# Kernel optimization log

Hardware: AMD Instinct MI355X
Metric: run time of the kernel (lower is better)

The kernel has to match this reference:

```python
import jax, jax.numpy as jnp
import numpy as np

B, L, D, H = 4, 8192, 512, 8


def _phi(x):
    # feature map: elu(x) + 1 (strictly positive)
    return jax.nn.elu(x) + 1.0


def setup_inputs() -> dict:
    key = jax.random.key(0)
    k1, k2, k3 = jax.random.split(key, 3)
    x = jax.random.normal(k1, (B, L, D), dtype=jnp.float32)
    w_qkv = jax.random.normal(k2, (D, 3 * D), dtype=jnp.float32) * 0.02
    b_qkv = jnp.zeros((3 * D,), dtype=jnp.float32)
    w_out = jax.random.normal(k3, (D, D), dtype=jnp.float32) * 0.02
    b_out = jnp.zeros((D,), dtype=jnp.float32)
    return {"x": x, "w_qkv": w_qkv, "b_qkv": b_qkv, "w_out": w_out,
            "b_out": b_out, "num_heads": H}


def reference(x, w_qkv, b_qkv, w_out, b_out, num_heads):
    Bx, Lx, Dx = x.shape
    dh = Dx // num_heads
    qkv = x @ w_qkv + b_qkv                       # (B, L, 3D)
    q, k, v = jnp.split(qkv, 3, axis=-1)
    # (B, L, D) -> (B, H, L, dh)
    def to_heads(t):
        return t.reshape(Bx, Lx, num_heads, dh).transpose(0, 2, 1, 3)
    q = _phi(to_heads(q))
    k = _phi(to_heads(k))
    v = to_heads(v)
    # kv[b,h,m,d] = sum_l k[b,h,l,d] * v[b,h,l,m]
    kv = jnp.einsum('bhld,bhlm->bhmd', k, v)      # (B, H, dh, dh)
    k_sum = jnp.sum(k, axis=2, keepdims=True)     # (B, H, 1, dh)
    # z[b,h,l,1] = 1 / <q_l, k_sum + 1e-6>
    z = 1.0 / jnp.einsum('bhld,bhmd->bhlm', q, k_sum + 1e-6)  # (B,H,L,1)
    out = jnp.einsum('bhld,bhmd->bhlm', q, kv) * z            # (B,H,L,dh)
    out = out.transpose(0, 2, 1, 3).reshape(Bx, Lx, Dx)
    return out @ w_out + b_out
```

## Files before the change

kernel.cpp:

```cpp
#include <hip/hip_runtime.h>
#include <hip/hip_bf16.h>
#include <math.h>

#define BB 4
#define LL 8192
#define DD 512
#define HH 8
#define MM (BB*LL)
#define NQKV 1536
#define CH 32

typedef __attribute__((ext_vector_type(4))) float f32x4;
typedef __attribute__((ext_vector_type(8))) short s16x8;
typedef __attribute__((ext_vector_type(4))) short s16x4;

__device__ __forceinline__ float bf2f(short u) {
  union { unsigned int i; float f; } c;
  c.i = ((unsigned int)(unsigned short)u) << 16;
  return c.f;
}
__device__ __forceinline__ short f2bf(float f) {
  union { float f; unsigned int i; } c; c.f = f;
  unsigned int r = c.i + 0x7FFFu + ((c.i >> 16) & 1u);
  return (short)(r >> 16);
}

__device__ __forceinline__ void gload16(const void* g, void* l) {
  __builtin_amdgcn_global_load_lds(
      (const __attribute__((address_space(1))) void*)(g),
      (__attribute__((address_space(3))) void*)(l), 16, 0, 0);
}

__global__ void conv_bf16(const float* __restrict__ in, short* __restrict__ out, int n) {
  int i = (blockIdx.x * blockDim.x + threadIdx.x) * 4;
  if (i < n) {
    float4 v = *reinterpret_cast<const float4*>(in + i);
    s16x4 o;
    o[0] = f2bf(v.x); o[1] = f2bf(v.y); o[2] = f2bf(v.z); o[3] = f2bf(v.w);
    *reinterpret_cast<s16x4*>(out + i) = o;
  }
}

__global__ void conv_wt(const float* __restrict__ w, short* __restrict__ wt, int K, int N) {
  int idx = blockIdx.x * blockDim.x + threadIdx.x;
  if (idx < K * N) {
    int n = idx / K, k = idx - n * K;
    wt[idx] = f2bf(w[(size_t)k * N + n]);
  }
}

template<int MODE>
__global__ __launch_bounds__(512, 4)
void gemm_bt(const short* __restrict__ A, const short* __restrict__ BT,
             const float* __restrict__ bias, void* __restrict__ Cout,
             short* __restrict__ ktb, short* __restrict__ vtb)
{
  constexpr int KD = 512;
  __shared__ __align__(16) char lds[65536];

  const int tid = threadIdx.x;
  const int wv = tid >> 6, lane = tid & 63;
  const int wm = wv >> 1, wn = wv & 1;
  const int fr = lane & 15, fq = lane >> 4;

  const int gx = gridDim.x;
  const int gy = gridDim.y;
  const int d = blockIdx.y * gx + blockIdx.x;
  const int nwg = gx * gy;
  const int lin = (d & 7) * (nwg >> 3) + (d >> 3);
  const int m0 = (lin / gy) * 256, n0 = (lin % gy) * 128;

  const int srow = tid >> 3;
  const int sunit = (tid & 7) ^ (srow & 7);
  const short* Ag = A  + (size_t)(m0 + srow) * KD + sunit * 8;
  const short* Bg = BT + (size_t)(n0 + srow) * KD + sunit * 8;
  char* ldsw = lds + wv * 1024;

  f32x4 acc[4][4] = {};

  for (int t = 0; t < 8; ++t) {
    const int k0 = t * 64;
#pragma unroll
    for (int i = 0; i < 4; ++i)
      gload16(Ag + (size_t)(i * 64) * KD + k0, ldsw + i * 8192);
#pragma unroll
    for (int i = 0; i < 2; ++i)
      gload16(Bg + (size_t)(i * 64) * KD + k0, ldsw + 32768 + i * 8192);
    __syncthreads();
#pragma unroll
    for (int kk = 0; kk < 2; ++kk) {
      s16x8 af[4], bfg[4];
#pragma unroll
      for (int i = 0; i < 4; ++i) {
        const int ra = wm * 64 + i * 16 + fr;
        const int ua = (kk * 4 + fq) ^ (ra & 7);
        af[i] = *(const s16x8*)(lds + ra * 128 + ua * 16);
      }
#pragma unroll
      for (int j = 0; j < 4; ++j) {
        const int rb = wn * 64 + j * 16 + fr;
        const int ub = (kk * 4 + fq) ^ (rb & 7);
        bfg[j] = *(const s16x8*)(lds + 32768 + rb * 128 + ub * 16);
      }
#pragma unroll
      for (int i = 0; i < 4; ++i)
#pragma unroll
        for (int j = 0; j < 4; ++j)
          acc[i][j] = __builtin_amdgcn_mfma_f32_16x16x32_bf16(af[i], bfg[j], acc[i][j], 0, 0, 0);
    }
    __syncthreads();
  }

  if (MODE == 0) {
    if (n0 < 512) {
      short* scr = (short*)lds;
#pragma unroll
      for (int j = 0; j < 4; ++j) {
        const int col = wn * 64 + j * 16 + fr;
        const float bv = bias[n0 + col];
#pragma unroll
        for (int i = 0; i < 4; ++i) {
          const int row = wm * 64 + i * 16 + fq * 4;
#pragma unroll
          for (int r = 0; r < 4; ++r) {
            float v = acc[i][j][r] + bv;
            v = (v > 0.f) ? (v + 1.f) : __expf(v);
            scr[(row + r) * 128 + col] = f2bf(v);
          }
        }
      }
      __syncthreads();
#pragma unroll
      for (int p = 0; p < 8; ++p) {
        const int off = p * 8192 + tid * 16;
        const int row = off >> 8, colb = off & 255;
        s16x8 v = *(const s16x8*)(lds + off);
        *(s16x8*)((short*)Cout + (size_t)(m0 + row) * 512 + n0 + (colb >> 1)) = v;
      }
    } else {
      const bool do_phi = (n0 < 1024);
      short* tdst = do_phi ? ktb : vtb;
      const int f0 = n0 - (do_phi ? 512 : 1024);
#pragma unroll
      for (int j = 0; j < 4; ++j) {
        const int col = wn * 64 + j * 16 + fr;
        const float bv = bias[n0 + col];
        const int cx = col & 31;
#pragma unroll
        for (int i = 0; i < 4; ++i) {
          const int l = wm * 64 + i * 16 + fq * 4;
          s16x4 pk;
#pragma unroll
          for (int r = 0; r < 4; ++r) {
            float v = acc[i][j][r] + bv;
            if (do_phi) v = (v > 0.f) ? (v + 1.f) : __expf(v);
            pk[r] = f2bf(v);
          }
          *(s16x4*)(lds + col * 512 + (((l >> 3) ^ cx) * 16) + (l & 7) * 2) = pk;
        }
      }
      __syncthreads();
#pragma unroll
      for (int p = 0; p < 8; ++p) {
        const int g = p * 512 + tid;
        const int col = g >> 5, up = g & 31;
        const int u = up ^ (col & 31);
        s16x8 v = *(const s16x8*)(lds + col * 512 + up * 16);
        const int f = f0 + col;
        const int hb = ((m0 >> 13) << 3) + (f >> 6);
        short* dst = tdst + ((size_t)hb * 64 + (f & 63)) * 8192 + (m0 & 8191) + u * 8;
        *(s16x8*)dst = v;
      }
    }
  } else {
    float* scrf = (float*)lds;
#pragma unroll
    for (int h = 0; h < 2; ++h) {
      __syncthreads();
      if ((wm >> 1) == h) {
#pragma unroll
        for (int j = 0; j < 4; ++j) {
          const int col = wn * 64 + j * 16 + fr;
          const float bv = bias[n0 + col];
#pragma unroll
          for (int i = 0; i < 4; ++i) {
            const int row = (wm & 1) * 64 + i * 16 + fq * 4;
#pragma unroll
            for (int r = 0; r < 4; ++r)
              scrf[(row + r) * 128 + col] = acc[i][j][r] + bv;
          }
        }
      }
      __syncthreads();
#pragma unroll
      for (int p = 0; p < 8; ++p) {
        const int off = p * 8192 + tid * 16;
        const int row = off >> 9, colb = off & 511;
        float4 v = *(const float4*)(lds + off);
        *(float4*)((float*)Cout + (size_t)(m0 + h * 128 + row) * 512 + n0 + (colb >> 2)) = v;
      }
    }
  }
}

__global__ __launch_bounds__(256, 4)
void kv_mfma(const short* __restrict__ kt, const short* __restrict__ vt,
             float* __restrict__ pkv, float* __restrict__ pks)
{
  const int hb = blockIdx.x, c = blockIdx.y;
  const int tid = threadIdx.x, wv = tid >> 6, lane = tid & 63;
  const int fr = lane & 15, fq = lane >> 4;
  const size_t base = (size_t)hb * 64 * 8192;
  const int l0 = c * 256;
  const short* vrow = vt + base + (size_t)fr * 8192 + l0 + fq * 8;
  const short* krow = kt + base + (size_t)(wv * 16 + fr) * 8192 + l0 + fq * 8;

  s16x8 ones;
#pragma unroll
  for (int j = 0; j < 8; ++j) ones[j] = (short)0x3F80;

  f32x4 acc[4] = {};
  f32x4 accd = {};
#pragma unroll
  for (int ks = 0; ks < 8; ++ks) {
    s16x8 bfr = *(const s16x8*)(krow + ks * 32);
    accd = __builtin_amdgcn_mfma_f32_16x16x32_bf16(ones, bfr, accd, 0, 0, 0);
#pragma unroll
    for (int i = 0; i < 4; ++i) {
      s16x8 af = *(const s16x8*)(vrow + (size_t)(i * 16) * 8192 + ks * 32);
      acc[i] = __builtin_amdgcn_mfma_f32_16x16x32_bf16(af, bfr, acc[i], 0, 0, 0);
    }
  }
  float* o = pkv + ((size_t)hb * CH + c) * 4096;
#pragma unroll
  for (int i = 0; i < 4; ++i)
#pragma unroll
    for (int r = 0; r < 4; ++r)
      o[(i * 16 + fq * 4 + r) * 64 + wv * 16 + fr] = acc[i][r];
  if (fq == 0)
    pks[((size_t)hb * CH + c) * 64 + wv * 16 + fr] = accd[0];
}

__global__ void kv_reduce(const float* __restrict__ pkv, const float* __restrict__ pks,
                          short* __restrict__ kv_b, short* __restrict__ ksum_b)
{
  const int idx = blockIdx.x * 256 + threadIdx.x;
  const int head = idx >> 12, md = idx & 4095;
  float s = 0.f;
  for (int i = 0; i < CH; ++i) s += pkv[((size_t)head * CH + i) * 4096 + md];
  kv_b[idx] = f2bf(s);
  if (md < 64) {
    float t = 0.f;
    for (int i = 0; i < CH; ++i) t += pks[((size_t)head * CH + i) * 64 + md];
    ksum_b[head * 64 + md] = f2bf(t + 1e-6f);
  }
}

__global__ __launch_bounds__(256, 2)
void attn_mfma(const short* __restrict__ q_b, const short* __restrict__ kv_b,
               const short* __restrict__ ksum_b, short* __restrict__ attn)
{
  const int hb = blockIdx.x;
  const int tile = blockIdx.y;
  const int b = hb >> 3, h = hb & 7;
  const int tid = threadIdx.x, wv = tid >> 6, lane = tid & 63;
  const int fr = lane & 15, fk = (lane >> 4) * 8;

  const short* kvp = kv_b + (size_t)hb * 4096;
  s16x8 bfrag[4][2];
#pragma unroll
  for (int j = 0; j < 4; ++j)
#pragma unroll
    for (int kk = 0; kk < 2; ++kk)
      bfrag[j][kk] = *(const s16x8*)(kvp + (j * 16 + fr) * 64 + kk * 32 + fk);
  s16x8 bden[2];
#pragma unroll
  for (int kk = 0; kk < 2; ++kk)
    bden[kk] = *(const s16x8*)(ksum_b + hb * 64 + kk * 32 + fk);

  const short* qb = q_b + (size_t)b * LL * DD + h * 64;
  const int l0 = tile * 256 + wv * 64;
  f32x4 accn[4][4] = {};
  f32x4 accd[4] = {};
#pragma unroll
  for (int i = 0; i < 4; ++i) {
#pragma unroll
    for (int kk = 0; kk < 2; ++kk) {
      s16x8 a = *(const s16x8*)(qb + (size_t)(l0 + i * 16 + fr) * DD + kk * 32 + fk);
      accd[i] = __builtin_amdgcn_mfma_f32_16x16x32_bf16(a, bden[kk], accd[i], 0, 0, 0);
#pragma unroll
      for (int j = 0; j < 4; ++j)
        accn[i][j] = __builtin_amdgcn_mfma_f32_16x16x32_bf16(a, bfrag[j][kk], accn[i][j], 0, 0, 0);
    }
  }

  short* ob = attn + (size_t)b * LL * DD + h * 64;
  const int fq = lane >> 4;
#pragma unroll
  for (int i = 0; i < 4; ++i) {
#pragma unroll
    for (int r = 0; r < 4; ++r) {
      const int row = l0 + i * 16 + fq * 4 + r;
      const float dinv = 1.0f / accd[i][r];
#pragma unroll
      for (int j = 0; j < 4; ++j) {
        ob[(size_t)row * DD + j * 16 + fr] = f2bf(accn[i][j][r] * dinv);
      }
    }
  }
}

extern "C" void kernel_launch(void* const* d_in, const int* in_sizes, int n_in,
                              void* d_out, int out_size, void* d_ws, size_t ws_size,
                              hipStream_t stream)
{
  const float* x     = (const float*)d_in[0];
  const float* w_qkv = (const float*)d_in[1];
  const float* b_qkv = (const float*)d_in[2];
  const float* w_out = (const float*)d_in[3];
  const float* b_out = (const float*)d_in[4];

  char* ws = (char*)d_ws;
  size_t off = 0;
  short* x_b   = (short*)(ws + off); off += (size_t)MM * DD * 2;
  short* wq_t  = (short*)(ws + off); off += (size_t)NQKV * DD * 2;
  short* wo_t  = (short*)(ws + off); off += (size_t)DD * DD * 2;
  short* q_b   = (short*)(ws + off); off += (size_t)MM * DD * 2;
  short* kt    = (short*)(ws + off); off += (size_t)32 * 64 * LL * 2;
  short* vt    = (short*)(ws + off); off += (size_t)32 * 64 * LL * 2;
  short* attn_b= (short*)(ws + off); off += (size_t)MM * DD * 2;
  float* pkv   = (float*)(ws + off); off += (size_t)32 * CH * 4096 * 4;
  float* pks   = (float*)(ws + off); off += (size_t)32 * CH * 64 * 4;
  short* kv_b  = (short*)(ws + off); off += (size_t)32 * 4096 * 2;
  short* ksum_b= (short*)(ws + off); off += (size_t)32 * 64 * 2;

  conv_bf16<<<dim3((MM * DD / 4 + 255) / 256), dim3(256), 0, stream>>>(x, x_b, MM * DD);
  conv_wt<<<dim3((DD * NQKV + 255) / 256), dim3(256), 0, stream>>>(w_qkv, wq_t, DD, NQKV);
  conv_wt<<<dim3((DD * DD + 255) / 256), dim3(256), 0, stream>>>(w_out, wo_t, DD, DD);

  gemm_bt<0><<<dim3(MM / 256, NQKV / 128), dim3(512), 0, stream>>>(
      x_b, wq_t, b_qkv, (void*)q_b, kt, vt);

  kv_mfma<<<dim3(32, CH), dim3(256), 0, stream>>>(kt, vt, pkv, pks);
  kv_reduce<<<dim3(512), dim3(256), 0, stream>>>(pkv, pks, kv_b, ksum_b);

  attn_mfma<<<dim3(32, 32), dim3(256), 0, stream>>>(q_b, kv_b, ksum_b, attn_b);

  gemm_bt<1><<<dim3(MM / 256, DD / 128), dim3(512), 0, stream>>>(
      attn_b, wo_t, b_out, d_out, nullptr, nullptr);
}
```

Measured before the change: 171.5 us.

## Enlarge GEMM tiles to 256x256 with a multi-stage LDS prefetch pipeline

```diff
diff --git a/kernel.cpp b/kernel.cpp
--- a/kernel.cpp
+++ b/kernel.cpp
@@ -50,64 +50,66 @@
 }
 
 template<int MODE>
-__global__ __launch_bounds__(512, 4)
-void gemm_bt(const short* __restrict__ A, const short* __restrict__ BT,
+__global__ __launch_bounds__(512, 2)
+void gemm256(const short* __restrict__ A, const short* __restrict__ BT,
              const float* __restrict__ bias, void* __restrict__ Cout,
              short* __restrict__ ktb, short* __restrict__ vtb)
 {
   constexpr int KD = 512;
-  __shared__ __align__(16) char lds[65536];
+  constexpr int NT = KD / 32;
+  __shared__ __align__(16) char lds[131072];
 
   const int tid = threadIdx.x;
   const int wv = tid >> 6, lane = tid & 63;
-  const int wm = wv >> 1, wn = wv & 1;
+  const int wm = wv >> 2, wn = wv & 3;
   const int fr = lane & 15, fq = lane >> 4;
 
-  const int gx = gridDim.x;
-  const int gy = gridDim.y;
+  const int gx = gridDim.x, gy = gridDim.y;
   const int d = blockIdx.y * gx + blockIdx.x;
   const int nwg = gx * gy;
   const int lin = (d & 7) * (nwg >> 3) + (d >> 3);
-  const int m0 = (lin / gy) * 256, n0 = (lin % gy) * 128;
-
-  const int srow = tid >> 3;
-  const int sunit = (tid & 7) ^ (srow & 7);
+  const int m0 = (lin / gy) * 256, n0 = (lin % gy) * 256;
+
+  const int srow = tid >> 2;
+  const int sunit = tid & 3;
   const short* Ag = A  + (size_t)(m0 + srow) * KD + sunit * 8;
   const short* Bg = BT + (size_t)(n0 + srow) * KD + sunit * 8;
   char* ldsw = lds + wv * 1024;
 
-  f32x4 acc[4][4] = {};
-
-  for (int t = 0; t < 8; ++t) {
-    const int k0 = t * 64;
-#pragma unroll
-    for (int i = 0; i < 4; ++i)
-      gload16(Ag + (size_t)(i * 64) * KD + k0, ldsw + i * 8192);
-#pragma unroll
-    for (int i = 0; i < 2; ++i)
-      gload16(Bg + (size_t)(i * 64) * KD + k0, ldsw + 32768 + i * 8192);
-    __syncthreads();
-#pragma unroll
-    for (int kk = 0; kk < 2; ++kk) {
-      s16x8 af[4], bfg[4];
-#pragma unroll
-      for (int i = 0; i < 4; ++i) {
-        const int ra = wm * 64 + i * 16 + fr;
-        const int ua = (kk * 4 + fq) ^ (ra & 7);
-        af[i] = *(const s16x8*)(lds + ra * 128 + ua * 16);
-      }
-#pragma unroll
-      for (int j = 0; j < 4; ++j) {
-        const int rb = wn * 64 + j * 16 + fr;
-        const int ub = (kk * 4 + fq) ^ (rb & 7);
-        bfg[j] = *(const s16x8*)(lds + 32768 + rb * 128 + ub * 16);
-      }
-#pragma unroll
-      for (int i = 0; i < 4; ++i)
-#pragma unroll
-        for (int j = 0; j < 4; ++j)
-          acc[i][j] = __builtin_amdgcn_mfma_f32_16x16x32_bf16(af[i], bfg[j], acc[i][j], 0, 0, 0);
-    }
+  auto stage = [&](int tn) {
+    const int sb = (tn & 3) * 32768;
+    const int k0 = tn * 32;
+    gload16(Ag + k0,                    ldsw + sb);
+    gload16(Ag + (size_t)128 * KD + k0, ldsw + sb + 8192);
+    gload16(Bg + k0,                    ldsw + sb + 16384);
+    gload16(Bg + (size_t)128 * KD + k0, ldsw + sb + 24576);
+  };
+
+  stage(0); stage(1);
+  asm volatile("s_waitcnt vmcnt(4)" ::: "memory");
+  __syncthreads();
+
+  f32x4 acc[8][4] = {};
+
+  for (int t = 0; t < NT; ++t) {
+    const int sb = (t & 3) * 32768;
+    if (t + 2 < NT) stage(t + 2);
+    const char* pa = lds + sb + (wm * 128 + fr) * 64 + fq * 16;
+    const char* pb = lds + sb + 16384 + (wn * 64 + fr) * 64 + fq * 16;
+    s16x8 bfr[4];
+#pragma unroll
+    for (int j = 0; j < 4; ++j) bfr[j] = *(const s16x8*)(pb + j * 1024);
+    __builtin_amdgcn_s_setprio(1);
+#pragma unroll
+    for (int i = 0; i < 8; ++i) {
+      s16x8 af = *(const s16x8*)(pa + i * 1024);
+#pragma unroll
+      for (int j = 0; j < 4; ++j)
+        acc[i][j] = __builtin_amdgcn_mfma_f32_16x16x32_bf16(af, bfr[j], acc[i][j], 0, 0, 0);
+    }
+    __builtin_amdgcn_s_setprio(0);
+    if (t < NT - 2)       asm volatile("s_waitcnt vmcnt(4)" ::: "memory");
+    else if (t == NT - 2) asm volatile("s_waitcnt vmcnt(0)" ::: "memory");
     __syncthreads();
   }
 
@@ -119,21 +121,21 @@
         const int col = wn * 64 + j * 16 + fr;
         const float bv = bias[n0 + col];
 #pragma unroll
-        for (int i = 0; i < 4; ++i) {
-          const int row = wm * 64 + i * 16 + fq * 4;
+        for (int i = 0; i < 8; ++i) {
+          const int row = wm * 128 + i * 16 + fq * 4;
 #pragma unroll
           for (int r = 0; r < 4; ++r) {
             float v = acc[i][j][r] + bv;
             v = (v > 0.f) ? (v + 1.f) : __expf(v);
-            scr[(row + r) * 128 + col] = f2bf(v);
+            scr[(row + r) * 256 + col] = f2bf(v);
           }
         }
       }
       __syncthreads();
 #pragma unroll
-      for (int p = 0; p < 8; ++p) {
+      for (int p = 0; p < 16; ++p) {
         const int off = p * 8192 + tid * 16;
-        const int row = off >> 8, colb = off & 255;
+        const int row = off >> 9, colb = off & 511;
         s16x8 v = *(const s16x8*)(lds + off);
         *(s16x8*)((short*)Cout + (size_t)(m0 + row) * 512 + n0 + (colb >> 1)) = v;
       }
@@ -147,8 +149,8 @@
         const float bv = bias[n0 + col];
         const int cx = col & 31;
 #pragma unroll
-        for (int i = 0; i < 4; ++i) {
-          const int l = wm * 64 + i * 16 + fq * 4;
+        for (int i = 0; i < 8; ++i) {
+          const int l = wm * 128 + i * 16 + fq * 4;
           s16x4 pk;
 #pragma unroll
           for (int r = 0; r < 4; ++r) {
@@ -161,7 +163,7 @@
       }
       __syncthreads();
 #pragma unroll
-      for (int p = 0; p < 8; ++p) {
+      for (int p = 0; p < 16; ++p) {
         const int g = p * 512 + tid;
         const int col = g >> 5, up = g & 31;
         const int u = up ^ (col & 31);
@@ -177,25 +179,25 @@
 #pragma unroll
     for (int h = 0; h < 2; ++h) {
       __syncthreads();
-      if ((wm >> 1) == h) {
+      if (wm == h) {
 #pragma unroll
         for (int j = 0; j < 4; ++j) {
           const int col = wn * 64 + j * 16 + fr;
           const float bv = bias[n0 + col];
 #pragma unroll
-          for (int i = 0; i < 4; ++i) {
-            const int row = (wm & 1) * 64 + i * 16 + fq * 4;
+          for (int i = 0; i < 8; ++i) {
+            const int row = i * 16 + fq * 4;
 #pragma unroll
             for (int r = 0; r < 4; ++r)
-              scrf[(row + r) * 128 + col] = acc[i][j][r] + bv;
+              scrf[(row + r) * 256 + col] = acc[i][j][r] + bv;
           }
         }
       }
       __syncthreads();
 #pragma unroll
-      for (int p = 0; p < 8; ++p) {
+      for (int p = 0; p < 16; ++p) {
         const int off = p * 8192 + tid * 16;
-        const int row = off >> 9, colb = off & 511;
+        const int row = off >> 10, colb = off & 1023;
         float4 v = *(const float4*)(lds + off);
         *(float4*)((float*)Cout + (size_t)(m0 + h * 128 + row) * 512 + n0 + (colb >> 2)) = v;
       }
@@ -338,7 +340,7 @@
   conv_wt<<<dim3((DD * NQKV + 255) / 256), dim3(256), 0, stream>>>(w_qkv, wq_t, DD, NQKV);
   conv_wt<<<dim3((DD * DD + 255) / 256), dim3(256), 0, stream>>>(w_out, wo_t, DD, DD);
 
-  gemm_bt<0><<<dim3(MM / 256, NQKV / 128), dim3(512), 0, stream>>>(
+  gemm256<0><<<dim3(MM / 256, NQKV / 256), dim3(512), 0, stream>>>(
       x_b, wq_t, b_qkv, (void*)q_b, kt, vt);
 
   kv_mfma<<<dim3(32, CH), dim3(256), 0, stream>>>(kt, vt, pkv, pks);
@@ -346,6 +348,6 @@
 
   attn_mfma<<<dim3(32, 32), dim3(256), 0, stream>>>(q_b, kv_b, ksum_b, attn_b);
 
-  gemm_bt<1><<<dim3(MM / 256, DD / 128), dim3(512), 0, stream>>>(
+  gemm256<1><<<dim3(MM / 256, DD / 256), dim3(512), 0, stream>>>(
       attn_b, wo_t, b_out, d_out, nullptr, nullptr);
 }
```

Result: slower. 183.5 us (+7.0%).

## Fuse attention application with output projection GEMM in one kernel

Applied to the files above, without the earlier changes.

```diff
diff --git a/kernel.cpp b/kernel.cpp
--- a/kernel.cpp
+++ b/kernel.cpp
@@ -172,34 +172,6 @@
         *(s16x8*)dst = v;
       }
     }
-  } else {
-    float* scrf = (float*)lds;
-#pragma unroll
-    for (int h = 0; h < 2; ++h) {
-      __syncthreads();
-      if ((wm >> 1) == h) {
-#pragma unroll
-        for (int j = 0; j < 4; ++j) {
-          const int col = wn * 64 + j * 16 + fr;
-          const float bv = bias[n0 + col];
-#pragma unroll
-          for (int i = 0; i < 4; ++i) {
-            const int row = (wm & 1) * 64 + i * 16 + fq * 4;
-#pragma unroll
-            for (int r = 0; r < 4; ++r)
-              scrf[(row + r) * 128 + col] = acc[i][j][r] + bv;
-          }
-        }
-      }
-      __syncthreads();
-#pragma unroll
-      for (int p = 0; p < 8; ++p) {
-        const int off = p * 8192 + tid * 16;
-        const int row = off >> 9, colb = off & 511;
-        float4 v = *(const float4*)(lds + off);
-        *(float4*)((float*)Cout + (size_t)(m0 + h * 128 + row) * 512 + n0 + (colb >> 2)) = v;
-      }
-    }
   }
 }
 
@@ -256,57 +228,105 @@
   }
 }
 
-__global__ __launch_bounds__(256, 2)
-void attn_mfma(const short* __restrict__ q_b, const short* __restrict__ kv_b,
-               const short* __restrict__ ksum_b, short* __restrict__ attn)
-{
-  const int hb = blockIdx.x;
-  const int tile = blockIdx.y;
-  const int b = hb >> 3, h = hb & 7;
-  const int tid = threadIdx.x, wv = tid >> 6, lane = tid & 63;
-  const int fr = lane & 15, fk = (lane >> 4) * 8;
-
-  const short* kvp = kv_b + (size_t)hb * 4096;
-  s16x8 bfrag[4][2];
-#pragma unroll
-  for (int j = 0; j < 4; ++j)
-#pragma unroll
-    for (int kk = 0; kk < 2; ++kk)
-      bfrag[j][kk] = *(const s16x8*)(kvp + (j * 16 + fr) * 64 + kk * 32 + fk);
-  s16x8 bden[2];
-#pragma unroll
-  for (int kk = 0; kk < 2; ++kk)
-    bden[kk] = *(const s16x8*)(ksum_b + hb * 64 + kk * 32 + fk);
-
-  const short* qb = q_b + (size_t)b * LL * DD + h * 64;
-  const int l0 = tile * 256 + wv * 64;
-  f32x4 accn[4][4] = {};
-  f32x4 accd[4] = {};
-#pragma unroll
-  for (int i = 0; i < 4; ++i) {
+__global__ __launch_bounds__(512, 4)
+void attn_out(const short* __restrict__ q_b, const short* __restrict__ kv_b,
+              const short* __restrict__ ksum_b, const short* __restrict__ wo_t,
+              const float* __restrict__ b_out, float* __restrict__ out)
+{
+  __shared__ __align__(16) char lds[65536];
+  const int tid = threadIdx.x;
+  const int wv = tid >> 6, lane = tid & 63;
+  const int fr = lane & 15, fq = lane >> 4;
+  const int l0 = blockIdx.x * 64;
+
+  {
+    const int hb = ((l0 >> 13) << 3) + wv;
+    const short* kvp = kv_b + (size_t)hb * 4096;
+    const short* ksp = ksum_b + hb * 64;
+    const short* qb = q_b + (size_t)l0 * 512 + wv * 64;
+
+    f32x4 accn[4][4] = {};
+    f32x4 accd[4] = {};
 #pragma unroll
     for (int kk = 0; kk < 2; ++kk) {
-      s16x8 a = *(const s16x8*)(qb + (size_t)(l0 + i * 16 + fr) * DD + kk * 32 + fk);
-      accd[i] = __builtin_amdgcn_mfma_f32_16x16x32_bf16(a, bden[kk], accd[i], 0, 0, 0);
+      s16x8 bfr[4], bden;
 #pragma unroll
       for (int j = 0; j < 4; ++j)
-        accn[i][j] = __builtin_amdgcn_mfma_f32_16x16x32_bf16(a, bfrag[j][kk], accn[i][j], 0, 0, 0);
-    }
-  }
-
-  short* ob = attn + (size_t)b * LL * DD + h * 64;
-  const int fq = lane >> 4;
-#pragma unroll
-  for (int i = 0; i < 4; ++i) {
-#pragma unroll
-    for (int r = 0; r < 4; ++r) {
-      const int row = l0 + i * 16 + fq * 4 + r;
-      const float dinv = 1.0f / accd[i][r];
-#pragma unroll
-      for (int j = 0; j < 4; ++j) {
-        ob[(size_t)row * DD + j * 16 + fr] = f2bf(accn[i][j][r] * dinv);
-      }
-    }
+        bfr[j] = *(const s16x8*)(kvp + (j * 16 + fr) * 64 + kk * 32 + fq * 8);
+      bden = *(const s16x8*)(ksp + kk * 32 + fq * 8);
+#pragma unroll
+      for (int i = 0; i < 4; ++i) {
+        s16x8 a = *(const s16x8*)(qb + (size_t)(i * 16 + fr) * 512 + kk * 32 + fq * 8);
+        accd[i] = __builtin_amdgcn_mfma_f32_16x16x32_bf16(a, bden, accd[i], 0, 0, 0);
+#pragma unroll
+        for (int j = 0; j < 4; ++j)
+          accn[i][j] = __builtin_amdgcn_mfma_f32_16x16x32_bf16(a, bfr[j], accn[i][j], 0, 0, 0);
+      }
+    }
+#pragma unroll
+    for (int i = 0; i < 4; ++i) {
+#pragma unroll
+      for (int r = 0; r < 4; ++r) {
+        const int row = i * 16 + fq * 4 + r;
+        const float dinv = 1.0f / accd[i][r];
+#pragma unroll
+        for (int j = 0; j < 4; ++j) {
+          const int col = wv * 64 + j * 16 + fr;
+          *(short*)(lds + row * 1024 + (((col >> 3) ^ (row & 7)) << 4) + ((col & 7) << 1))
+              = f2bf(accn[i][j][r] * dinv);
+        }
+      }
+    }
+  }
+  __syncthreads();
+
+  const int wm = wv >> 2, wn = wv & 3;
+  f32x4 acc[2][8] = {};
+  for (int kt = 0; kt < 16; ++kt) {
+    s16x8 af[2];
+#pragma unroll
+    for (int i = 0; i < 2; ++i) {
+      const int row = wm * 32 + i * 16 + fr;
+      const int u = (kt * 4 + fq) ^ (row & 7);
+      af[i] = *(const s16x8*)(lds + row * 1024 + u * 16);
+    }
+#pragma unroll
+    for (int j = 0; j < 8; ++j) {
+      const int n = wn * 128 + j * 16 + fr;
+      s16x8 bfw = *(const s16x8*)(wo_t + (size_t)n * 512 + kt * 32 + fq * 8);
+#pragma unroll
+      for (int i = 0; i < 2; ++i)
+        acc[i][j] = __builtin_amdgcn_mfma_f32_16x16x32_bf16(af[i], bfw, acc[i][j], 0, 0, 0);
+    }
+  }
+  __syncthreads();
+
+  float* scrf = (float*)lds;
+#pragma unroll
+  for (int h = 0; h < 2; ++h) {
+    if (wm == h) {
+#pragma unroll
+      for (int j = 0; j < 8; ++j) {
+        const int col = wn * 128 + j * 16 + fr;
+        const float bv = b_out[col];
+#pragma unroll
+        for (int i = 0; i < 2; ++i) {
+          const int row = i * 16 + fq * 4;
+#pragma unroll
+          for (int r = 0; r < 4; ++r)
+            scrf[(row + r) * 512 + col] = acc[i][j][r] + bv;
+        }
+      }
+    }
+    __syncthreads();
+#pragma unroll
+    for (int p = 0; p < 8; ++p) {
+      const int off = p * 8192 + tid * 16;
+      const int row = off >> 11, colb = off & 2047;
+      float4 v = *(const float4*)(lds + off);
+      *(float4*)(out + (size_t)(l0 + h * 32 + row) * 512 + (colb >> 2)) = v;
+    }
+    __syncthreads();
   }
 }
 
@@ -328,7 +348,6 @@
   short* q_b   = (short*)(ws + off); off += (size_t)MM * DD * 2;
   short* kt    = (short*)(ws + off); off += (size_t)32 * 64 * LL * 2;
   short* vt    = (short*)(ws + off); off += (size_t)32 * 64 * LL * 2;
-  short* attn_b= (short*)(ws + off); off += (size_t)MM * DD * 2;
   float* pkv   = (float*)(ws + off); off += (size_t)32 * CH * 4096 * 4;
   float* pks   = (float*)(ws + off); off += (size_t)32 * CH * 64 * 4;
   short* kv_b  = (short*)(ws + off); off += (size_t)32 * 4096 * 2;
@@ -344,8 +363,6 @@
   kv_mfma<<<dim3(32, CH), dim3(256), 0, stream>>>(kt, vt, pkv, pks);
   kv_reduce<<<dim3(512), dim3(256), 0, stream>>>(pkv, pks, kv_b, ksum_b);
 
-  attn_mfma<<<dim3(32, 32), dim3(256), 0, stream>>>(q_b, kv_b, ksum_b, attn_b);
-
-  gemm_bt<1><<<dim3(MM / 256, DD / 128), dim3(512), 0, stream>>>(
-      attn_b, wo_t, b_out, d_out, nullptr, nullptr);
-}
+  attn_out<<<dim3(MM / 64), dim3(512), 0, stream>>>(
+      q_b, kv_b, ksum_b, wo_t, b_out, (float*)d_out);
+}
```

Measured after the change: 212.6 us. 24.0% more time.
